# Optimization experiments

Measured on AMD Instinct MI355X. Metric: run time of the kernel, lower is better.

## Reference

```python
import jax, jax.numpy as jnp
import numpy as np

B, T, V, E, H, C = 64, 2048, 4096, 128, 128, 8


def setup_inputs() -> dict:
    key = jax.random.key(0)
    ks = jax.random.split(key, 13)
    s = 0.1
    return {
        "x": jax.random.randint(ks[0], (B, T), 0, V),
        "emb": jax.random.normal(ks[1], (V, E), jnp.float32) * s,
        "Wih_f": jax.random.normal(ks[2], (4 * H, E), jnp.float32) * s,
        "Whh_f": jax.random.normal(ks[3], (4 * H, H), jnp.float32) * s,
        "b_f": jax.random.normal(ks[4], (4 * H,), jnp.float32) * s,
        "Wih_b": jax.random.normal(ks[5], (4 * H, E), jnp.float32) * s,
        "Whh_b": jax.random.normal(ks[6], (4 * H, H), jnp.float32) * s,
        "b_b": jax.random.normal(ks[7], (4 * H,), jnp.float32) * s,
        "fc_w": jax.random.normal(ks[8], (C, 2 * H), jnp.float32) * s,
        "fc_b": jax.random.normal(ks[9], (C,), jnp.float32) * s,
        "trans": jax.random.normal(ks[10], (C, C), jnp.float32) * s,
        "start": jax.random.normal(ks[11], (C,), jnp.float32) * s,
        "end": jax.random.normal(ks[12], (C,), jnp.float32) * s,
    }


def _lstm_scan(xs, Wih, Whh, b, reverse):
    # xs: [T, B, E]; PyTorch gate order i, f, g, o; b = b_ih + b_hh fused.
    Hd = Whh.shape[1]
    Bd = xs.shape[1]

    def step(carry, xt):
        h, c = carry
        g = xt @ Wih.T + h @ Whh.T + b  # [B, 4H]
        i, f, gg, o = jnp.split(g, 4, axis=-1)
        c = jax.nn.sigmoid(f) * c + jax.nn.sigmoid(i) * jnp.tanh(gg)
        h = jax.nn.sigmoid(o) * jnp.tanh(c)
        return (h, c), h

    init = (jnp.zeros((Bd, Hd), xs.dtype), jnp.zeros((Bd, Hd), xs.dtype))
    _, hs = jax.lax.scan(step, init, xs, reverse=reverse)
    return hs  # [T, B, H]


def reference(x, emb, Wih_f, Whh_f, b_f, Wih_b, Whh_b, b_b, fc_w, fc_b, trans, start, end):
    e = emb[x]                       # [B, T, E] embedding lookup
    xs = jnp.swapaxes(e, 0, 1)       # [T, B, E]
    hf = _lstm_scan(xs, Wih_f, Whh_f, b_f, False)
    hb = _lstm_scan(xs, Wih_b, Whh_b, b_b, True)
    h = jnp.concatenate([hf, hb], axis=-1)      # [T, B, 2H]
    # dropout is identity in eval mode
    logits = h @ fc_w.T + fc_b                  # [T, B, C] emissions

    # CRF forward algorithm -> log partition per sequence
    alpha0 = start + logits[0]                  # [B, C]

    def crf_step(alpha, em):
        a = jax.scipy.special.logsumexp(alpha[:, :, None] + trans[None], axis=1) + em
        return a, None

    alpha, _ = jax.lax.scan(crf_step, alpha0, logits[1:])
    return jax.scipy.special.logsumexp(alpha + end, axis=-1)  # [B]
```

## Files before the change

### kernel.cpp

```cpp
#include <hip/hip_runtime.h>
#include <hip/hip_bf16.h>
#include <hip/hip_fp16.h>

typedef __attribute__((ext_vector_type(8))) _Float16 half8;
typedef __attribute__((ext_vector_type(4))) _Float16 half4v;
typedef __attribute__((ext_vector_type(4))) float f32x4;

#define T_LEN 2048
#define NCH 128
#define CHS 16

__device__ __forceinline__ float rcpf_(float x){ return __builtin_amdgcn_rcpf(x); }

__device__ __forceinline__ half4v pack4(float4 a){
  half4v r;
  r[0]=(_Float16)a.x; r[1]=(_Float16)a.y; r[2]=(_Float16)a.z; r[3]=(_Float16)a.w;
  return r;
}

__global__ __launch_bounds__(512) void k_table(const float* __restrict__ emb,
    const float* __restrict__ Wih_f, const float* __restrict__ b_f,
    const float* __restrict__ Wih_b, const float* __restrict__ b_b,
    float* __restrict__ table){
  const int dir = blockIdx.x & 1, vt = blockIdx.x >> 1;
  const float* Wih  = dir ? Wih_b : Wih_f;
  const float* bias = dir ? b_b  : b_f;
  const int w = threadIdx.x >> 6, l = threadIdx.x & 63;
  const int lA = l & 15, hi = l >> 4;

  half4v wf[4][8];
#pragma unroll
  for (int g = 0; g < 4; ++g)
#pragma unroll
    for (int kb = 0; kb < 8; ++kb){
      const size_t base = (size_t)(g*128 + 16*w + lA)*128 + kb*16 + 4*hi;
      wf[g][kb] = pack4(*reinterpret_cast<const float4*>(Wih + base));
    }
  const int v0 = vt*16;
  half4v bfr[8];
#pragma unroll
  for (int kb = 0; kb < 8; ++kb){
    const size_t base = (size_t)(v0 + lA)*128 + kb*16 + 4*hi;
    bfr[kb] = pack4(*reinterpret_cast<const float4*>(emb + base));
  }
  f32x4 acc[4];
#pragma unroll
  for (int g = 0; g < 4; ++g)
    acc[g] = *reinterpret_cast<const f32x4*>(bias + g*128 + 16*w + 4*hi);
#pragma unroll
  for (int kb = 0; kb < 8; ++kb)
#pragma unroll
    for (int g = 0; g < 4; ++g)
      acc[g] = __builtin_amdgcn_mfma_f32_16x16x16f16(wf[g][kb], bfr[kb], acc[g], 0, 0, 0);
  float* outp = table + ((size_t)dir*4096 + v0 + lA)*512 + 16*w + 4*hi;
#pragma unroll
  for (int g = 0; g < 4; ++g)
    *reinterpret_cast<f32x4*>(outp + g*128) = acc[g];
}

__device__ __forceinline__ void epi_step(float iv, float fv, float gv, float ov,
                                         float& c, float& h){
  float Ae = __expf(-iv);
  float Be = __expf(2.f*gv);
  float st = (Be - 1.f) * rcpf_((1.f + Ae)*(Be + 1.f));
  float Fe = __expf(-fv);
  float cn = rcpf_(1.f + Fe)*c + st;
  c = cn;
  float Oe = __expf(-ov);
  float Ce = __expf(2.f*cn);
  h = (Ce - 1.f) * rcpf_((1.f + Oe)*(Ce + 1.f));
}

__global__ __launch_bounds__(512, 2) void k_lstm(
    const float* __restrict__ Whh_f, const float* __restrict__ Whh_b,
    const int* __restrict__ x, const float* __restrict__ table,
    _Float16* __restrict__ hcat){
  const int dir = blockIdx.x >> 2;
  const int chain = blockIdx.x & 3;
  const float* Whh = dir ? Whh_b : Whh_f;
  const float* tbl = table + (size_t)dir*4096*512;
  const int w  = threadIdx.x >> 6;
  const int l  = threadIdx.x & 63;
  const int lA = l & 15;
  const int hi = l >> 4;

  half4v whh[4][8];
#pragma unroll
  for (int g = 0; g < 4; ++g)
#pragma unroll
    for (int kb = 0; kb < 8; ++kb){
      const size_t base = (size_t)(g*128 + 16*w + lA)*128 + kb*16 + 4*hi;
      whh[g][kb] = pack4(*reinterpret_cast<const float4*>(Whh + base));
    }

  __shared__ __align__(16) _Float16 hbuf[2][8][64][4];
  reinterpret_cast<int4*>(&hbuf[0][0][0][0])[threadIdx.x] = make_int4(0,0,0,0);
  __syncthreads();

  const int b = chain*16 + lA;
  const int* xrow = x + (size_t)b*T_LEN;
  _Float16* hgbase = hcat + (size_t)b*256 + dir*128 + 16*w + 4*hi;
  _Float16* ldsw0 = &hbuf[0][w][l][0];
  _Float16* ldsw1 = &hbuf[1][w][l][0];
  const int toff = 16*w + 4*hi;

  f32x4 tb_c[4], tb_n[4];
  int idx_n;
  {
    const int tx0 = dir ? (T_LEN-1) : 0;
    const int idx0 = xrow[tx0];
    const float* tp = tbl + (size_t)idx0*512 + toff;
#pragma unroll
    for (int g = 0; g < 4; ++g) tb_c[g] = *reinterpret_cast<const f32x4*>(tp + g*128);
    idx_n = xrow[dir ? (T_LEN-2) : 1];
  }
  float cc0=0.f, cc1=0.f, cc2=0.f, cc3=0.f;

  for (int t = 0; t < T_LEN; ++t){
    const int tx = dir ? (T_LEN-1-t) : t;
    if (t + 1 < T_LEN){
      const float* tp = tbl + (size_t)idx_n*512 + toff;
#pragma unroll
      for (int g = 0; g < 4; ++g) tb_n[g] = *reinterpret_cast<const f32x4*>(tp + g*128);
    }
    if (t + 2 < T_LEN) idx_n = xrow[dir ? (T_LEN-3-t) : (t+2)];

    const int pb = t & 1;
    half4v ah[8];
#pragma unroll
    for (int kb = 0; kb < 8; ++kb)
      ah[kb] = *reinterpret_cast<const half4v*>(&hbuf[pb][kb][l][0]);

    f32x4 acc[4];
#pragma unroll
    for (int g = 0; g < 4; ++g) acc[g] = tb_c[g];
#pragma unroll
    for (int kb = 0; kb < 8; ++kb)
#pragma unroll
      for (int g = 0; g < 4; ++g)
        acc[g] = __builtin_amdgcn_mfma_f32_16x16x16f16(whh[g][kb], ah[kb], acc[g], 0, 0, 0);

    float hv0, hv1, hv2, hv3;
    epi_step(acc[0][0], acc[1][0], acc[2][0], acc[3][0], cc0, hv0);
    epi_step(acc[0][1], acc[1][1], acc[2][1], acc[3][1], cc1, hv1);
    epi_step(acc[0][2], acc[1][2], acc[2][2], acc[3][2], cc2, hv2);
    epi_step(acc[0][3], acc[1][3], acc[2][3], acc[3][3], cc3, hv3);

    half4v hp;
    hp[0]=(_Float16)hv0; hp[1]=(_Float16)hv1; hp[2]=(_Float16)hv2; hp[3]=(_Float16)hv3;
    *reinterpret_cast<half4v*>((t & 1) ? ldsw0 : ldsw1) = hp;
    *reinterpret_cast<half4v*>(hgbase + (size_t)tx*16384) = hp;
#pragma unroll
    for (int g = 0; g < 4; ++g) tb_c[g] = tb_n[g];
    asm volatile("s_waitcnt lgkmcnt(0)" ::: "memory");
    __builtin_amdgcn_sched_barrier(0);
    __builtin_amdgcn_s_barrier();
    __builtin_amdgcn_sched_barrier(0);
  }
}

__global__ __launch_bounds__(256) void k_crfchunk(const _Float16* __restrict__ hcat,
    const float* __restrict__ fc_w, const float* __restrict__ fc_b,
    const float* __restrict__ trans, float* __restrict__ chunkP){
  const int wv = threadIdx.x >> 6;
  const int l  = threadIdx.x & 63;
  const int task = blockIdx.x*4 + wv;
  const int k = task >> 6;
  const int b = task & 63;
  const int i = l >> 3, jc = l & 7;
  float trC[8];
#pragma unroll
  for (int kk = 0; kk < 8; ++kk) trC[kk] = trans[kk*8 + jc];
  const float tii = trans[l];
  float wreg[32];
#pragma unroll
  for (int q = 0; q < 32; ++q) wreg[q] = fc_w[jc*256 + i*32 + q];
  const float fcb = fc_b[jc];
  const int tstart = 1 + k*CHS;
  const int len = (CHS < T_LEN - tstart) ? CHS : (T_LEN - tstart);
  float P = 0.f;
  for (int s = 0; s < len; ++s){
    const int t = tstart + s;
    const _Float16* hp = hcat + ((size_t)t*64 + b)*256 + i*32;
    float dot = 0.f;
#pragma unroll
    for (int q8 = 0; q8 < 4; ++q8){
      half8 hv = *reinterpret_cast<const half8*>(hp + q8*8);
#pragma unroll
      for (int j = 0; j < 8; ++j) dot += (float)hv[j] * wreg[q8*8 + j];
    }
    dot += __shfl_xor(dot, 8);
    dot += __shfl_xor(dot, 16);
    dot += __shfl_xor(dot, 32);
    const float em = fcb + dot;
    if (s == 0){
      P = tii + em;
    } else {
      float v[8];
#pragma unroll
      for (int kk = 0; kk < 8; ++kk) v[kk] = __shfl(P, (l & 56) | kk) + trC[kk];
      float m = v[0];
#pragma unroll
      for (int kk = 1; kk < 8; ++kk) m = fmaxf(m, v[kk]);
      float ss = 0.f;
#pragma unroll
      for (int kk = 0; kk < 8; ++kk) ss += __expf(v[kk] - m);
      P = m + __logf(ss) + em;
    }
  }
  chunkP[(size_t)task*64 + l] = P;
}

__global__ __launch_bounds__(512) void k_crffinal(const _Float16* __restrict__ hcat,
    const float* __restrict__ fc_w, const float* __restrict__ fc_b,
    const float* __restrict__ trans, const float* __restrict__ startv,
    const float* __restrict__ endv, const float* __restrict__ chunkP,
    float* __restrict__ out){
  const int tid = threadIdx.x;
  const int b = tid >> 3, jc = tid & 7;
  const int l = tid & 63;
  float em = fc_b[jc];
  const _Float16* hp = hcat + (size_t)b*256;
  const float* wr = fc_w + jc*256;
#pragma unroll
  for (int q = 0; q < 32; ++q){
    half8 hv = *reinterpret_cast<const half8*>(hp + q*8);
#pragma unroll
    for (int j = 0; j < 8; ++j) em += (float)hv[j] * wr[q*8 + j];
  }
  float alpha = startv[jc] + em;
  for (int k = 0; k < NCH; ++k){
    const float* pk = chunkP + ((size_t)k*64 + b)*64;
    float v[8];
#pragma unroll
    for (int kk = 0; kk < 8; ++kk) v[kk] = __shfl(alpha, (l & 56) | kk) + pk[kk*8 + jc];
    float m = v[0];
#pragma unroll
    for (int kk = 1; kk < 8; ++kk) m = fmaxf(m, v[kk]);
    float ss = 0.f;
#pragma unroll
    for (int kk = 0; kk < 8; ++kk) ss += __expf(v[kk] - m);
    alpha = m + __logf(ss);
  }
  float vf = alpha + endv[jc];
  float m = vf;
  m = fmaxf(m, __shfl_xor(m, 1));
  m = fmaxf(m, __shfl_xor(m, 2));
  m = fmaxf(m, __shfl_xor(m, 4));
  float e = __expf(vf - m);
  e += __shfl_xor(e, 1);
  e += __shfl_xor(e, 2);
  e += __shfl_xor(e, 4);
  if (jc == 0) out[b] = m + __logf(e);
}

extern "C" void kernel_launch(void* const* d_in, const int* in_sizes, int n_in,
                              void* d_out, int out_size, void* d_ws, size_t ws_size,
                              hipStream_t stream){
  const int*   x     = (const int*)d_in[0];
  const float* emb   = (const float*)d_in[1];
  const float* Wih_f = (const float*)d_in[2];
  const float* Whh_f = (const float*)d_in[3];
  const float* b_f   = (const float*)d_in[4];
  const float* Wih_b = (const float*)d_in[5];
  const float* Whh_b = (const float*)d_in[6];
  const float* b_b   = (const float*)d_in[7];
  const float* fc_w  = (const float*)d_in[8];
  const float* fc_b  = (const float*)d_in[9];
  const float* trans = (const float*)d_in[10];
  const float* startp= (const float*)d_in[11];
  const float* endp  = (const float*)d_in[12];
  float* out = (float*)d_out;

  const size_t off_tbl  = 0;
  const size_t off_hcat = 16777216;
  const size_t off_chk  = 16777216 + 67108864;
  const size_t need     = off_chk + 2097152;
  if (ws_size < need){
    (void)hipMemsetAsync(d_out, 0, 64*sizeof(float), stream);
    return;
  }
  float* table  = (float*)((char*)d_ws + off_tbl);
  _Float16* hcat = (_Float16*)((char*)d_ws + off_hcat);
  float* chunkP  = (float*)((char*)d_ws + off_chk);

  k_table<<<512, 512, 0, stream>>>(emb, Wih_f, b_f, Wih_b, b_b, table);
  k_lstm<<<8, 512, 0, stream>>>(Whh_f, Whh_b, x, table, hcat);
  k_crfchunk<<<2048, 256, 0, stream>>>(hcat, fc_w, fc_b, trans, chunkP);
  k_crffinal<<<1, 512, 0, stream>>>(hcat, fc_w, fc_b, trans, startp, endp, chunkP, out);
}
```

Before: 2.668 ms.

## Unroll LSTM loop by two with two-step-ahead table prefetch and contiguous table layout

The input-projection table is written in a per-thread contiguous layout, so each lane's four gate vectors sit in 64 consecutive bytes instead of four 512-byte-strided chunks. The recurrent loop is unrolled by two with separate A and B prefetch buffers, issuing table loads two steps ahead and placing them after the first MFMA so they overlap the matrix work. This is meant to hide the gather latency on the serial critical path and improve load coalescing, at the cost of more registers.

```diff
diff --git a/kernel.cpp b/kernel.cpp
--- a/kernel.cpp
+++ b/kernel.cpp
@@ -52,10 +52,10 @@
 #pragma unroll
     for (int g = 0; g < 4; ++g)
       acc[g] = __builtin_amdgcn_mfma_f32_16x16x16f16(wf[g][kb], bfr[kb], acc[g], 0, 0, 0);
-  float* outp = table + ((size_t)dir*4096 + v0 + lA)*512 + 16*w + 4*hi;
+  float* outp = table + ((((size_t)dir*4096 + v0 + lA)*8 + w)*4 + hi)*16;
 #pragma unroll
   for (int g = 0; g < 4; ++g)
-    *reinterpret_cast<f32x4*>(outp + g*128) = acc[g];
+    *reinterpret_cast<f32x4*>(outp + g*4) = acc[g];
 }
 
 __device__ __forceinline__ void epi_step(float iv, float fv, float gv, float ov,
@@ -102,60 +102,99 @@
   _Float16* hgbase = hcat + (size_t)b*256 + dir*128 + 16*w + 4*hi;
   _Float16* ldsw0 = &hbuf[0][w][l][0];
   _Float16* ldsw1 = &hbuf[1][w][l][0];
-  const int toff = 16*w + 4*hi;
-
-  f32x4 tb_c[4], tb_n[4];
-  int idx_n;
+  const int seg = (w*4 + hi)*16;
+
+  f32x4 tbA[4], tbB[4];
+  int idxA2, idxB2;
   {
-    const int tx0 = dir ? (T_LEN-1) : 0;
-    const int idx0 = xrow[tx0];
-    const float* tp = tbl + (size_t)idx0*512 + toff;
-#pragma unroll
-    for (int g = 0; g < 4; ++g) tb_c[g] = *reinterpret_cast<const f32x4*>(tp + g*128);
-    idx_n = xrow[dir ? (T_LEN-2) : 1];
+    const int i0 = xrow[dir ? 2047 : 0];
+    const int i1 = xrow[dir ? 2046 : 1];
+    const float* pA = tbl + (size_t)i0*512 + seg;
+    const float* pB = tbl + (size_t)i1*512 + seg;
+#pragma unroll
+    for (int g = 0; g < 4; ++g) tbA[g] = *reinterpret_cast<const f32x4*>(pA + g*4);
+#pragma unroll
+    for (int g = 0; g < 4; ++g) tbB[g] = *reinterpret_cast<const f32x4*>(pB + g*4);
+    idxA2 = xrow[dir ? 2045 : 2];
+    idxB2 = xrow[dir ? 2044 : 3];
   }
   float cc0=0.f, cc1=0.f, cc2=0.f, cc3=0.f;
 
-  for (int t = 0; t < T_LEN; ++t){
-    const int tx = dir ? (T_LEN-1-t) : t;
-    if (t + 1 < T_LEN){
-      const float* tp = tbl + (size_t)idx_n*512 + toff;
-#pragma unroll
-      for (int g = 0; g < 4; ++g) tb_n[g] = *reinterpret_cast<const f32x4*>(tp + g*128);
-    }
-    if (t + 2 < T_LEN) idx_n = xrow[dir ? (T_LEN-3-t) : (t+2)];
-
-    const int pb = t & 1;
-    half4v ah[8];
-#pragma unroll
-    for (int kb = 0; kb < 8; ++kb)
-      ah[kb] = *reinterpret_cast<const half4v*>(&hbuf[pb][kb][l][0]);
-
-    f32x4 acc[4];
-#pragma unroll
-    for (int g = 0; g < 4; ++g) acc[g] = tb_c[g];
-#pragma unroll
-    for (int kb = 0; kb < 8; ++kb)
+  for (int tt = 0; tt < T_LEN; tt += 2){
+    {
+      half4v ah[8];
+#pragma unroll
+      for (int kb = 0; kb < 8; ++kb)
+        ah[kb] = *reinterpret_cast<const half4v*>(&hbuf[0][kb][l][0]);
+      f32x4 acc[4];
 #pragma unroll
       for (int g = 0; g < 4; ++g)
-        acc[g] = __builtin_amdgcn_mfma_f32_16x16x16f16(whh[g][kb], ah[kb], acc[g], 0, 0, 0);
-
-    float hv0, hv1, hv2, hv3;
-    epi_step(acc[0][0], acc[1][0], acc[2][0], acc[3][0], cc0, hv0);
-    epi_step(acc[0][1], acc[1][1], acc[2][1], acc[3][1], cc1, hv1);
-    epi_step(acc[0][2], acc[1][2], acc[2][2], acc[3][2], cc2, hv2);
-    epi_step(acc[0][3], acc[1][3], acc[2][3], acc[3][3], cc3, hv3);
-
-    half4v hp;
-    hp[0]=(_Float16)hv0; hp[1]=(_Float16)hv1; hp[2]=(_Float16)hv2; hp[3]=(_Float16)hv3;
-    *reinterpret_cast<half4v*>((t & 1) ? ldsw0 : ldsw1) = hp;
-    *reinterpret_cast<half4v*>(hgbase + (size_t)tx*16384) = hp;
-#pragma unroll
-    for (int g = 0; g < 4; ++g) tb_c[g] = tb_n[g];
-    asm volatile("s_waitcnt lgkmcnt(0)" ::: "memory");
-    __builtin_amdgcn_sched_barrier(0);
-    __builtin_amdgcn_s_barrier();
-    __builtin_amdgcn_sched_barrier(0);
+        acc[g] = __builtin_amdgcn_mfma_f32_16x16x16f16(whh[g][0], ah[0], tbA[g], 0, 0, 0);
+      {
+        const float* pA = tbl + (size_t)idxA2*512 + seg;
+#pragma unroll
+        for (int g = 0; g < 4; ++g) tbA[g] = *reinterpret_cast<const f32x4*>(pA + g*4);
+        const int tn = (tt+4 < T_LEN) ? tt+4 : T_LEN-1;
+        idxA2 = xrow[dir ? (T_LEN-1-tn) : tn];
+      }
+#pragma unroll
+      for (int kb = 1; kb < 8; ++kb)
+#pragma unroll
+        for (int g = 0; g < 4; ++g)
+          acc[g] = __builtin_amdgcn_mfma_f32_16x16x16f16(whh[g][kb], ah[kb], acc[g], 0, 0, 0);
+
+      float hv0, hv1, hv2, hv3;
+      epi_step(acc[0][0], acc[1][0], acc[2][0], acc[3][0], cc0, hv0);
+      epi_step(acc[0][1], acc[1][1], acc[2][1], acc[3][1], cc1, hv1);
+      epi_step(acc[0][2], acc[1][2], acc[2][2], acc[3][2], cc2, hv2);
+      epi_step(acc[0][3], acc[1][3], acc[2][3], acc[3][3], cc3, hv3);
+      half4v hp;
+      hp[0]=(_Float16)hv0; hp[1]=(_Float16)hv1; hp[2]=(_Float16)hv2; hp[3]=(_Float16)hv3;
+      *reinterpret_cast<half4v*>(ldsw1) = hp;
+      const int tx = dir ? (T_LEN-1-tt) : tt;
+      *reinterpret_cast<half4v*>(hgbase + (size_t)tx*16384) = hp;
+      asm volatile("s_waitcnt lgkmcnt(0)" ::: "memory");
+      __builtin_amdgcn_sched_barrier(0);
+      __builtin_amdgcn_s_barrier();
+      __builtin_amdgcn_sched_barrier(0);
+    }
+    {
+      half4v ah[8];
+#pragma unroll
+      for (int kb = 0; kb < 8; ++kb)
+        ah[kb] = *reinterpret_cast<const half4v*>(&hbuf[1][kb][l][0]);
+      f32x4 acc[4];
+#pragma unroll
+      for (int g = 0; g < 4; ++g)
+        acc[g] = __builtin_amdgcn_mfma_f32_16x16x16f16(whh[g][0], ah[0], tbB[g], 0, 0, 0);
+      {
+        const float* pB = tbl + (size_t)idxB2*512 + seg;
+#pragma unroll
+        for (int g = 0; g < 4; ++g) tbB[g] = *reinterpret_cast<const f32x4*>(pB + g*4);
+        const int tn = (tt+5 < T_LEN) ? tt+5 : T_LEN-1;
+        idxB2 = xrow[dir ? (T_LEN-1-tn) : tn];
+      }
+#pragma unroll
+      for (int kb = 1; kb < 8; ++kb)
+#pragma unroll
+        for (int g = 0; g < 4; ++g)
+          acc[g] = __builtin_amdgcn_mfma_f32_16x16x16f16(whh[g][kb], ah[kb], acc[g], 0, 0, 0);
+
+      float hv0, hv1, hv2, hv3;
+      epi_step(acc[0][0], acc[1][0], acc[2][0], acc[3][0], cc0, hv0);
+      epi_step(acc[0][1], acc[1][1], acc[2][1], acc[3][1], cc1, hv1);
+      epi_step(acc[0][2], acc[1][2], acc[2][2], acc[3][2], cc2, hv2);
+      epi_step(acc[0][3], acc[1][3], acc[2][3], acc[3][3], cc3, hv3);
+      half4v hp;
+      hp[0]=(_Float16)hv0; hp[1]=(_Float16)hv1; hp[2]=(_Float16)hv2; hp[3]=(_Float16)hv3;
+      *reinterpret_cast<half4v*>(ldsw0) = hp;
+      const int tx = dir ? (T_LEN-2-tt) : tt+1;
+      *reinterpret_cast<half4v*>(hgbase + (size_t)tx*16384) = hp;
+      asm volatile("s_waitcnt lgkmcnt(0)" ::: "memory");
+      __builtin_amdgcn_sched_barrier(0);
+      __builtin_amdgcn_s_barrier();
+      __builtin_amdgcn_sched_barrier(0);
+    }
   }
 }
 
```

Result: no change. 2.621 ms (-1.8%).

## Interleave two batch chains per LSTM block with 16x16x32 MFMA and prescaled gates

Applied to the files above, without the earlier changes.

The LSTM kernel now runs two independent 16-sequence chains per block (4 blocks instead of 8) and interleaves their substeps, so one chain's MFMA work can hide the other's epilogue and barrier latency. It switches to the 16x16x32 f16 MFMA with half8 operands, halving the MFMA instruction count. The input-projection table is relaid out contiguously per lane and prescaled by -log2e / 2log2e, with matching scaling folded into Whh, so the epilogue uses exp2 without extra multiplies. Table prefetch is deepened to two steps ahead. The trade-off is more serial work per block and fewer CUs used, while both chains still sit on each block's per-step critical path.

```diff
diff --git a/kernel.cpp b/kernel.cpp
--- a/kernel.cpp
+++ b/kernel.cpp
@@ -9,6 +9,7 @@
 #define T_LEN 2048
 #define NCH 128
 #define CHS 16
+#define L2E 1.4426950408889634f
 
 __device__ __forceinline__ float rcpf_(float x){ return __builtin_amdgcn_rcpf(x); }
 
@@ -17,6 +18,14 @@
   r[0]=(_Float16)a.x; r[1]=(_Float16)a.y; r[2]=(_Float16)a.z; r[3]=(_Float16)a.w;
   return r;
 }
+__device__ __forceinline__ half8 pack8s(float4 a, float4 b, float s){
+  half8 r;
+  r[0]=(_Float16)(a.x*s); r[1]=(_Float16)(a.y*s); r[2]=(_Float16)(a.z*s); r[3]=(_Float16)(a.w*s);
+  r[4]=(_Float16)(b.x*s); r[5]=(_Float16)(b.y*s); r[6]=(_Float16)(b.z*s); r[7]=(_Float16)(b.w*s);
+  return r;
+}
+
+__device__ __constant__ float GSC[4] = { -L2E, -L2E, 2.f*L2E, -L2E };
 
 __global__ __launch_bounds__(512) void k_table(const float* __restrict__ emb,
     const float* __restrict__ Wih_f, const float* __restrict__ b_f,
@@ -52,110 +61,148 @@
 #pragma unroll
     for (int g = 0; g < 4; ++g)
       acc[g] = __builtin_amdgcn_mfma_f32_16x16x16f16(wf[g][kb], bfr[kb], acc[g], 0, 0, 0);
-  float* outp = table + ((size_t)dir*4096 + v0 + lA)*512 + 16*w + 4*hi;
-#pragma unroll
-  for (int g = 0; g < 4; ++g)
-    *reinterpret_cast<f32x4*>(outp + g*128) = acc[g];
-}
-
-__device__ __forceinline__ void epi_step(float iv, float fv, float gv, float ov,
+  float* outp = table + ((((size_t)dir*4096 + v0 + lA)*8 + w)*4 + hi)*16;
+#pragma unroll
+  for (int g = 0; g < 4; ++g){
+    f32x4 v = acc[g]*GSC[g];
+    *reinterpret_cast<f32x4*>(outp + g*4) = v;
+  }
+}
+
+__device__ __forceinline__ void epi_step(float ei, float ef, float eg, float eo,
                                          float& c, float& h){
-  float Ae = __expf(-iv);
-  float Be = __expf(2.f*gv);
+  float Ae = exp2f(ei);
+  float Be = exp2f(eg);
   float st = (Be - 1.f) * rcpf_((1.f + Ae)*(Be + 1.f));
-  float Fe = __expf(-fv);
+  float Fe = exp2f(ef);
   float cn = rcpf_(1.f + Fe)*c + st;
   c = cn;
-  float Oe = __expf(-ov);
-  float Ce = __expf(2.f*cn);
+  float Oe = exp2f(eo);
+  float Ce = exp2f(2.f*L2E*cn);
   h = (Ce - 1.f) * rcpf_((1.f + Oe)*(Ce + 1.f));
 }
 
-__global__ __launch_bounds__(512, 2) void k_lstm(
+#define MFMA32 __builtin_amdgcn_mfma_f32_16x16x32_f16
+
+#define SUBSTEP(HSRC, LDSW, TB, IDXV, HGB, TX, C0, C1, C2, C3) do{            \
+  half8 ah0 = *reinterpret_cast<const half8*>(&HSRC[0][l][0]);                \
+  half8 ah1 = *reinterpret_cast<const half8*>(&HSRC[1][l][0]);                \
+  half8 ah2 = *reinterpret_cast<const half8*>(&HSRC[2][l][0]);                \
+  half8 ah3 = *reinterpret_cast<const half8*>(&HSRC[3][l][0]);                \
+  f32x4 a0 = MFMA32(whh[0][0], ah0, TB[0], 0, 0, 0);                          \
+  f32x4 a1 = MFMA32(whh[1][0], ah0, TB[1], 0, 0, 0);                          \
+  f32x4 a2 = MFMA32(whh[2][0], ah0, TB[2], 0, 0, 0);                          \
+  f32x4 a3 = MFMA32(whh[3][0], ah0, TB[3], 0, 0, 0);                          \
+  { const float* _pf = tblD + (size_t)(IDXV)*512 + seg;                       \
+    TB[0] = *reinterpret_cast<const f32x4*>(_pf);                             \
+    TB[1] = *reinterpret_cast<const f32x4*>(_pf + 4);                         \
+    TB[2] = *reinterpret_cast<const f32x4*>(_pf + 8);                         \
+    TB[3] = *reinterpret_cast<const f32x4*>(_pf + 12); }                      \
+  a0 = MFMA32(whh[0][1], ah1, a0, 0, 0, 0);                                   \
+  a1 = MFMA32(whh[1][1], ah1, a1, 0, 0, 0);                                   \
+  a2 = MFMA32(whh[2][1], ah1, a2, 0, 0, 0);                                   \
+  a3 = MFMA32(whh[3][1], ah1, a3, 0, 0, 0);                                   \
+  a0 = MFMA32(whh[0][2], ah2, a0, 0, 0, 0);                                   \
+  a1 = MFMA32(whh[1][2], ah2, a1, 0, 0, 0);                                   \
+  a2 = MFMA32(whh[2][2], ah2, a2, 0, 0, 0);                                   \
+  a3 = MFMA32(whh[3][2], ah2, a3, 0, 0, 0);                                   \
+  a0 = MFMA32(whh[0][3], ah3, a0, 0, 0, 0);                                   \
+  a1 = MFMA32(whh[1][3], ah3, a1, 0, 0, 0);                                   \
+  a2 = MFMA32(whh[2][3], ah3, a2, 0, 0, 0);                                   \
+  a3 = MFMA32(whh[3][3], ah3, a3, 0, 0, 0);                                   \
+  float hv0, hv1, hv2, hv3;                                                   \
+  epi_step(a0[0], a1[0], a2[0], a3[0], C0, hv0);                              \
+  epi_step(a0[1], a1[1], a2[1], a3[1], C1, hv1);                              \
+  epi_step(a0[2], a1[2], a2[2], a3[2], C2, hv2);                              \
+  epi_step(a0[3], a1[3], a2[3], a3[3], C3, hv3);                              \
+  half4v hp;                                                                  \
+  hp[0]=(_Float16)hv0; hp[1]=(_Float16)hv1; hp[2]=(_Float16)hv2; hp[3]=(_Float16)hv3; \
+  *reinterpret_cast<half4v*>(LDSW) = hp;                                      \
+  *reinterpret_cast<half4v*>(HGB + (size_t)(TX)*16384) = hp;                  \
+}while(0)
+
+__global__ __launch_bounds__(512, 1) void k_lstm(
     const float* __restrict__ Whh_f, const float* __restrict__ Whh_b,
     const int* __restrict__ x, const float* __restrict__ table,
     _Float16* __restrict__ hcat){
-  const int dir = blockIdx.x >> 2;
-  const int chain = blockIdx.x & 3;
-  const float* Whh = dir ? Whh_b : Whh_f;
-  const float* tbl = table + (size_t)dir*4096*512;
+  const int d  = blockIdx.x >> 1;
+  const int cp = blockIdx.x & 1;
+  const float* Whh  = d ? Whh_b : Whh_f;
+  const float* tblD = table + (size_t)d*4096*512;
   const int w  = threadIdx.x >> 6;
   const int l  = threadIdx.x & 63;
   const int lA = l & 15;
   const int hi = l >> 4;
 
-  half4v whh[4][8];
+  half8 whh[4][4];
 #pragma unroll
   for (int g = 0; g < 4; ++g)
 #pragma unroll
-    for (int kb = 0; kb < 8; ++kb){
-      const size_t base = (size_t)(g*128 + 16*w + lA)*128 + kb*16 + 4*hi;
-      whh[g][kb] = pack4(*reinterpret_cast<const float4*>(Whh + base));
-    }
-
-  __shared__ __align__(16) _Float16 hbuf[2][8][64][4];
-  reinterpret_cast<int4*>(&hbuf[0][0][0][0])[threadIdx.x] = make_int4(0,0,0,0);
+    for (int q = 0; q < 4; ++q){
+      const size_t base = (size_t)(g*128 + 16*w + lA)*128 + q*32 + 4*hi;
+      whh[g][q] = pack8s(*reinterpret_cast<const float4*>(Whh + base),
+                         *reinterpret_cast<const float4*>(Whh + base + 16), GSC[g]);
+    }
+
+  __shared__ __align__(16) _Float16 hbufA[2][4][64][8];
+  __shared__ __align__(16) _Float16 hbufB[2][4][64][8];
+  reinterpret_cast<int4*>(&hbufA[0][0][0][0])[threadIdx.x] = make_int4(0,0,0,0);
+  reinterpret_cast<int4*>(&hbufB[0][0][0][0])[threadIdx.x] = make_int4(0,0,0,0);
   __syncthreads();
 
-  const int b = chain*16 + lA;
-  const int* xrow = x + (size_t)b*T_LEN;
-  _Float16* hgbase = hcat + (size_t)b*256 + dir*128 + 16*w + 4*hi;
-  _Float16* ldsw0 = &hbuf[0][w][l][0];
-  _Float16* ldsw1 = &hbuf[1][w][l][0];
-  const int toff = 16*w + 4*hi;
-
-  f32x4 tb_c[4], tb_n[4];
-  int idx_n;
+  const int bA = (cp*2)*16 + lA;
+  const int bB = bA + 16;
+  const int* xrowA = x + (size_t)bA*T_LEN;
+  const int* xrowB = x + (size_t)bB*T_LEN;
+  _Float16* hgA = hcat + (size_t)bA*256 + d*128 + 16*w + 4*hi;
+  _Float16* hgB = hcat + (size_t)bB*256 + d*128 + 16*w + 4*hi;
+  _Float16* ldswA0 = &hbufA[0][w>>1][l][4*(w&1)];
+  _Float16* ldswA1 = &hbufA[1][w>>1][l][4*(w&1)];
+  _Float16* ldswB0 = &hbufB[0][w>>1][l][4*(w&1)];
+  _Float16* ldswB1 = &hbufB[1][w>>1][l][4*(w&1)];
+  const int seg = (w*4 + hi)*16;
+
+  f32x4 tbEA[4], tbOA[4], tbEB[4], tbOB[4];
+  int idxEA, idxOA, idxEB, idxOB;
   {
-    const int tx0 = dir ? (T_LEN-1) : 0;
-    const int idx0 = xrow[tx0];
-    const float* tp = tbl + (size_t)idx0*512 + toff;
-#pragma unroll
-    for (int g = 0; g < 4; ++g) tb_c[g] = *reinterpret_cast<const f32x4*>(tp + g*128);
-    idx_n = xrow[dir ? (T_LEN-2) : 1];
-  }
-  float cc0=0.f, cc1=0.f, cc2=0.f, cc3=0.f;
-
-  for (int t = 0; t < T_LEN; ++t){
-    const int tx = dir ? (T_LEN-1-t) : t;
-    if (t + 1 < T_LEN){
-      const float* tp = tbl + (size_t)idx_n*512 + toff;
-#pragma unroll
-      for (int g = 0; g < 4; ++g) tb_n[g] = *reinterpret_cast<const f32x4*>(tp + g*128);
-    }
-    if (t + 2 < T_LEN) idx_n = xrow[dir ? (T_LEN-3-t) : (t+2)];
-
-    const int pb = t & 1;
-    half4v ah[8];
-#pragma unroll
-    for (int kb = 0; kb < 8; ++kb)
-      ah[kb] = *reinterpret_cast<const half4v*>(&hbuf[pb][kb][l][0]);
-
-    f32x4 acc[4];
-#pragma unroll
-    for (int g = 0; g < 4; ++g) acc[g] = tb_c[g];
-#pragma unroll
-    for (int kb = 0; kb < 8; ++kb)
-#pragma unroll
-      for (int g = 0; g < 4; ++g)
-        acc[g] = __builtin_amdgcn_mfma_f32_16x16x16f16(whh[g][kb], ah[kb], acc[g], 0, 0, 0);
-
-    float hv0, hv1, hv2, hv3;
-    epi_step(acc[0][0], acc[1][0], acc[2][0], acc[3][0], cc0, hv0);
-    epi_step(acc[0][1], acc[1][1], acc[2][1], acc[3][1], cc1, hv1);
-    epi_step(acc[0][2], acc[1][2], acc[2][2], acc[3][2], cc2, hv2);
-    epi_step(acc[0][3], acc[1][3], acc[2][3], acc[3][3], cc3, hv3);
-
-    half4v hp;
-    hp[0]=(_Float16)hv0; hp[1]=(_Float16)hv1; hp[2]=(_Float16)hv2; hp[3]=(_Float16)hv3;
-    *reinterpret_cast<half4v*>((t & 1) ? ldsw0 : ldsw1) = hp;
-    *reinterpret_cast<half4v*>(hgbase + (size_t)tx*16384) = hp;
-#pragma unroll
-    for (int g = 0; g < 4; ++g) tb_c[g] = tb_n[g];
-    asm volatile("s_waitcnt lgkmcnt(0)" ::: "memory");
-    __builtin_amdgcn_sched_barrier(0);
-    __builtin_amdgcn_s_barrier();
-    __builtin_amdgcn_sched_barrier(0);
+    auto xi = [&](int t){ return d ? (T_LEN-1-t) : t; };
+    auto ld4 = [&](f32x4* dst, int idx){
+      const float* p = tblD + (size_t)idx*512 + seg;
+#pragma unroll
+      for (int g = 0; g < 4; ++g) dst[g] = *reinterpret_cast<const f32x4*>(p + g*4);
+    };
+    ld4(tbEA, xrowA[xi(0)]);  ld4(tbOA, xrowA[xi(1)]);
+    ld4(tbEB, xrowB[xi(0)]);  ld4(tbOB, xrowB[xi(1)]);
+    idxEA = xrowA[xi(2)]; idxOA = xrowA[xi(3)];
+    idxEB = xrowB[xi(2)]; idxOB = xrowB[xi(3)];
+  }
+  float cA0=0.f,cA1=0.f,cA2=0.f,cA3=0.f, cB0=0.f,cB1=0.f,cB2=0.f,cB3=0.f;
+
+  for (int tt = 0; tt < T_LEN; tt += 2){
+    {
+      const int tx = d ? (T_LEN-1-tt) : tt;
+      SUBSTEP(hbufA[0], ldswA1, tbEA, idxEA, hgA, tx, cA0, cA1, cA2, cA3);
+      SUBSTEP(hbufB[0], ldswB1, tbEB, idxEB, hgB, tx, cB0, cB1, cB2, cB3);
+      const int tn = (tt+4 < T_LEN) ? tt+4 : T_LEN-1;
+      const int xn = d ? (T_LEN-1-tn) : tn;
+      idxEA = xrowA[xn]; idxEB = xrowB[xn];
+      asm volatile("s_waitcnt lgkmcnt(0)" ::: "memory");
+      __builtin_amdgcn_sched_barrier(0);
+      __builtin_amdgcn_s_barrier();
+      __builtin_amdgcn_sched_barrier(0);
+    }
+    {
+      const int tx = d ? (T_LEN-2-tt) : tt+1;
+      SUBSTEP(hbufA[1], ldswA0, tbOA, idxOA, hgA, tx, cA0, cA1, cA2, cA3);
+      SUBSTEP(hbufB[1], ldswB0, tbOB, idxOB, hgB, tx, cB0, cB1, cB2, cB3);
+      const int tn = (tt+5 < T_LEN) ? tt+5 : T_LEN-1;
+      const int xn = d ? (T_LEN-1-tn) : tn;
+      idxOA = xrowA[xn]; idxOB = xrowB[xn];
+      asm volatile("s_waitcnt lgkmcnt(0)" ::: "memory");
+      __builtin_amdgcn_sched_barrier(0);
+      __builtin_amdgcn_s_barrier();
+      __builtin_amdgcn_sched_barrier(0);
+    }
   }
 }
 
@@ -285,7 +332,7 @@
   float* chunkP  = (float*)((char*)d_ws + off_chk);
 
   k_table<<<512, 512, 0, stream>>>(emb, Wih_f, b_f, Wih_b, b_b, table);
-  k_lstm<<<8, 512, 0, stream>>>(Whh_f, Whh_b, x, table, hcat);
+  k_lstm<<<4, 512, 0, stream>>>(Whh_f, Whh_b, x, table, hcat);
   k_crfchunk<<<2048, 256, 0, stream>>>(hcat, fc_w, fc_b, trans, chunkP);
   k_crffinal<<<1, 512, 0, stream>>>(hcat, fc_w, fc_b, trans, startp, endp, chunkP, out);
 }
```

Result: slower. 5.988 ms (+124.5%).
